# Performance work log

Hardware: AMD Instinct MI355X
Metric: run time of the kernel (lower is better)

The kernel has to match this reference:

```python
import jax, jax.numpy as jnp
import numpy as np

WINDOW = 512  # sliding-window size (keys per query, including self)


def setup_inputs() -> dict:
    key = jax.random.key(0)
    ks = jax.random.split(key, 5)
    B, T, C = 2, 8192, 1024
    s = 1.0 / np.sqrt(C)
    return {
        "x": jax.random.normal(ks[0], (B, T, C), dtype=jnp.float32),
        "Wq": jax.random.normal(ks[1], (C, C), dtype=jnp.float32) * s,
        "Wk": jax.random.normal(ks[2], (C, C), dtype=jnp.float32) * s,
        "Wv": jax.random.normal(ks[3], (C, C), dtype=jnp.float32) * s,
        "Wo": jax.random.normal(ks[4], (C, C), dtype=jnp.float32) * s,
    }


def _block_local_attn(q, k, v, window):
    # q,k,v: [B,H,T,D]; causal sliding-window attention, honoring sparsity by
    # attending only to the current and previous block of size `window`.
    B, H, T, D = q.shape
    W = window
    nb = T // W
    scale = 1.0 / jnp.sqrt(jnp.asarray(D, q.dtype))
    qb = q.reshape(B, H, nb, W, D)
    kb = k.reshape(B, H, nb, W, D)
    vb = v.reshape(B, H, nb, W, D)
    # previous block (zero-padded for block 0)
    kp = jnp.pad(kb, ((0, 0), (0, 0), (1, 0), (0, 0), (0, 0)))[:, :, :nb]
    vp = jnp.pad(vb, ((0, 0), (0, 0), (1, 0), (0, 0), (0, 0)))[:, :, :nb]
    k2 = jnp.concatenate([kp, kb], axis=3)  # [B,H,nb,2W,D]
    v2 = jnp.concatenate([vp, vb], axis=3)
    i = jnp.arange(W)[:, None]          # query index within block
    j = jnp.arange(2 * W)[None, :]      # key index (0..W-1 prev, W..2W-1 cur)
    # key global offset = j - W relative to query block start; causal window of
    # size W (self + W-1 previous) <=> i < j <= i + W
    base = (j > i) & (j <= i + W)                                  # [W,2W]
    prev_ok = (jnp.arange(nb)[:, None] > 0) | (jnp.arange(2 * W)[None, :] >= W)
    mask = base[None, :, :] & prev_ok[:, None, :]                  # [nb,W,2W]
    scores = jnp.einsum("bhnqd,bhnkd->bhnqk", qb, k2) * scale
    scores = jnp.where(mask[None, None], scores, jnp.asarray(-1e30, scores.dtype))
    p = jax.nn.softmax(scores, axis=-1)
    out = jnp.einsum("bhnqk,bhnkd->bhnqd", p, v2)
    return out.reshape(B, H, T, D)


def reference(x, Wq, Wk, Wv, Wo):
    B, T, C = x.shape
    H = 16
    D = C // H
    # nn.Linear(y = x @ W^T), bias=False
    q = (x @ Wq.T).reshape(B, T, H, D).transpose(0, 2, 1, 3)
    k = (x @ Wk.T).reshape(B, T, H, D).transpose(0, 2, 1, 3)
    v = (x @ Wv.T).reshape(B, T, H, D).transpose(0, 2, 1, 3)
    out = _block_local_attn(q, k, v, WINDOW)
    out = out.transpose(0, 2, 1, 3).reshape(B, T, C)
    return out @ Wo.T
```

## Files before the change

kernel.cpp:

```cpp
#include <hip/hip_runtime.h>
#include <hip/hip_bf16.h>
#include <stdint.h>

typedef __attribute__((ext_vector_type(8))) short short8;
typedef __attribute__((ext_vector_type(4))) float f32x4;
typedef __hip_bfloat16 bf16;

#define AS1 __attribute__((address_space(1)))
#define AS3 __attribute__((address_space(3)))

__device__ __forceinline__ void gl16(const void* g, void* l) {
  __builtin_amdgcn_global_load_lds((const AS1 unsigned int*)g,
                                   (AS3 unsigned int*)l, 16, 0, 0);
}

__device__ __forceinline__ unsigned short bfbits(float x) {
  union { bf16 b; unsigned short u; } c; c.b = __float2bfloat16(x); return c.u;
}

#define SCHED0 __builtin_amdgcn_sched_barrier(0)

__global__ __launch_bounds__(256) void k_cvt(const float* __restrict__ src,
                                             bf16* __restrict__ dst, int n8) {
  int i = blockIdx.x * blockDim.x + threadIdx.x;
  int stride = gridDim.x * blockDim.x;
  for (; i < n8; i += stride) {
    const float4* p = (const float4*)src + (size_t)i * 2;
    float4 a = p[0], b = p[1];
    bf16 tmp[8];
    tmp[0] = __float2bfloat16(a.x); tmp[1] = __float2bfloat16(a.y);
    tmp[2] = __float2bfloat16(a.z); tmp[3] = __float2bfloat16(a.w);
    tmp[4] = __float2bfloat16(b.x); tmp[5] = __float2bfloat16(b.y);
    tmp[6] = __float2bfloat16(b.z); tmp[7] = __float2bfloat16(b.w);
    *(short8*)(dst + (size_t)i * 8) = *(short8*)tmp;
  }
}

__global__ __launch_bounds__(256) void k_cvtw(
    const float* __restrict__ w0, const float* __restrict__ w1,
    const float* __restrict__ w2, const float* __restrict__ w3,
    bf16* __restrict__ d0, bf16* __restrict__ d1,
    bf16* __restrict__ d2, bf16* __restrict__ d3) {
  int gi = blockIdx.x * 256 + threadIdx.x;
  int m = gi >> 17;
  int i = gi & 131071;
  const float* src = (m == 0) ? w0 : (m == 1) ? w1 : (m == 2) ? w2 : w3;
  bf16* dst = (m == 0) ? d0 : (m == 1) ? d1 : (m == 2) ? d2 : d3;
  const float4* p = (const float4*)src + (size_t)i * 2;
  float4 a = p[0], b = p[1];
  bf16 tmp[8];
  tmp[0] = __float2bfloat16(a.x); tmp[1] = __float2bfloat16(a.y);
  tmp[2] = __float2bfloat16(a.z); tmp[3] = __float2bfloat16(a.w);
  tmp[4] = __float2bfloat16(b.x); tmp[5] = __float2bfloat16(b.y);
  tmp[6] = __float2bfloat16(b.z); tmp[7] = __float2bfloat16(b.w);
  *(short8*)(dst + (size_t)i * 8) = *(short8*)tmp;
}


#define GEMM_BODY(...)                                                         \
  const int Kd = 1024;                                                         \
  const int nk = 32;                                              \
  __shared__ bf16 As[4][256 * 32];                                             \
  __shared__ bf16 Bs[4][256 * 32];                                             \
  int tid = threadIdx.x;                                                       \
  int lane = tid & 63, wid = tid >> 6;                                         \
  int l15 = lane & 15, hi = lane >> 4;                                         \
  int wm = wid >> 2, wn = wid & 3;                                             \
  f32x4 acc[8][4];                                                             \
  _Pragma("unroll") for (int i = 0; i < 8; i++)                                \
      _Pragma("unroll") for (int j = 0; j < 4; j++)                            \
          acc[i][j] = (f32x4){0.f, 0.f, 0.f, 0.f};                             \
  auto stageA = [&](int slot, int kk) {                                        \
    const bf16* ab = Abase + kk * 32;                                          \
    _Pragma("unroll") for (int pass = 0; pass < 2; pass++) {                   \
      int p = pass * 512 + tid;                                                \
      int row = p >> 2;                                                        \
      int u = (p & 3) ^ ((row >> 1) & 3);                                      \
      gl16(ab + (size_t)row * Kd + u * 8, (char*)(&As[slot][0]) + p * 16);     \
    }                                                                          \
  };                                                                           \
  auto stageB = [&](int slot, int kk) {                                        \
    const bf16* bb = Bbase + kk * 32;                                          \
    _Pragma("unroll") for (int pass = 0; pass < 2; pass++) {                   \
      int p = pass * 512 + tid;                                                \
      int row = p >> 2;                                                        \
      int u = (p & 3) ^ ((row >> 1) & 3);                                      \
      gl16(bb + (size_t)row * Kd + u * 8, (char*)(&Bs[slot][0]) + p * 16);     \
    }                                                                          \
  };                                                                           \
  stageA(0, 0); stageB(0, 0);                                                  \
  stageA(1, 1); stageB(1, 1);                                                  \
  stageA(2, 2); stageB(2, 2);                                                  \
  asm volatile("s_waitcnt vmcnt(8)" ::: "memory");                             \
  SCHED0; __builtin_amdgcn_s_barrier(); SCHED0;                                \
  int sw = ((l15 >> 1) & 3) << 4;                                              \
  int arow = wm * 128 + l15;                                                   \
  int brow = wn * 64 + l15;                                                    \
  short8 ax[4], ahi[4], bcur[4], axn[4], bn[4];                                \
  _Pragma("unroll") for (int mf = 0; mf < 4; mf++)                             \
      ax[mf] = *(const short8*)((const char*)(&As[0][0]) +                     \
                                (((arow + mf * 16) * 64 + hi * 16) ^ sw));     \
  _Pragma("unroll") for (int nf = 0; nf < 4; nf++)                             \
      bcur[nf] = *(const short8*)((const char*)(&Bs[0][0]) +                   \
                                  (((brow + nf * 16) * 64 + hi * 16) ^ sw));   \
  _Pragma("unroll 2") for (int t = 0; t < nk; ++t) {                           \
    int s = t & 3, sn = (t + 1) & 3;                                           \
    const char* Ab = (const char*)(&As[s][0]);                                 \
    _Pragma("unroll") for (int mf = 0; mf < 4; mf++)                           \
        ahi[mf] = *(const short8*)(Ab +                                        \
            (((arow + 64 + mf * 16) * 64 + hi * 16) ^ sw));                    \
    if (t + 3 < nk) stageA((t + 3) & 3, t + 3);                                \
    SCHED0;                                                                    \
    __builtin_amdgcn_s_setprio(1);                                             \
    _Pragma("unroll") for (int mf = 0; mf < 4; mf++)                           \
        _Pragma("unroll") for (int nf = 0; nf < 4; nf++)                       \
            acc[mf][nf] = __builtin_amdgcn_mfma_f32_16x16x32_bf16(             \
                ax[mf], bcur[nf], acc[mf][nf], 0, 0, 0);                       \
    __builtin_amdgcn_s_setprio(0);                                             \
    SCHED0;                                                                    \
    if (t + 1 < nk) {                                                          \
      if (t + 3 < nk)      asm volatile("s_waitcnt vmcnt(6)" ::: "memory");    \
      else if (t + 2 < nk) asm volatile("s_waitcnt vmcnt(4)" ::: "memory");    \
      else                 asm volatile("s_waitcnt vmcnt(0)" ::: "memory");    \
      SCHED0; __builtin_amdgcn_s_barrier(); SCHED0;                            \
      if (t + 3 < nk) stageB((t + 3) & 3, t + 3);                              \
      const char* AbN = (const char*)(&As[sn][0]);                             \
      const char* BbN = (const char*)(&Bs[sn][0]);                             \
      _Pragma("unroll") for (int mf = 0; mf < 4; mf++)                         \
          axn[mf] = *(const short8*)(AbN +                                     \
              (((arow + mf * 16) * 64 + hi * 16) ^ sw));                       \
      _Pragma("unroll") for (int nf = 0; nf < 4; nf++)                         \
          bn[nf] = *(const short8*)(BbN +                                      \
              (((brow + nf * 16) * 64 + hi * 16) ^ sw));                       \
      SCHED0;                                                                  \
    }                                                                          \
    __builtin_amdgcn_s_setprio(1);                                             \
    _Pragma("unroll") for (int mf = 0; mf < 4; mf++)                           \
        _Pragma("unroll") for (int nf = 0; nf < 4; nf++)                       \
            acc[mf + 4][nf] = __builtin_amdgcn_mfma_f32_16x16x32_bf16(         \
                ahi[mf], bcur[nf], acc[mf + 4][nf], 0, 0, 0);                  \
    __builtin_amdgcn_s_setprio(0);                                             \
    SCHED0;                                                                    \
    if (t + 1 < nk) {                                                          \
      __builtin_amdgcn_s_barrier(); SCHED0;                                    \
      _Pragma("unroll") for (int i = 0; i < 4; i++) {                          \
        ax[i] = axn[i]; bcur[i] = bn[i];                                       \
      }                                                                        \
    }                                                                          \
  }                                                                            \
  __VA_ARGS__

__global__ __launch_bounds__(512, 2) void k_qkv_gemm(
    const bf16* __restrict__ X, const bf16* __restrict__ Wq,
    const bf16* __restrict__ Wk, const bf16* __restrict__ Wv,
    bf16* __restrict__ Q, bf16* __restrict__ K, bf16* __restrict__ V) {
  int bid = blockIdx.x;
  int wsel = bid >> 8;
  int rem = bid & 255;
  int mt = rem & 63;
  int nt = rem >> 6;
  const bf16* W = (wsel == 0) ? Wq : (wsel == 1) ? Wk : Wv;
  bf16* Dst = (wsel == 0) ? Q : (wsel == 1) ? K : V;
  const bf16* Abase = X + (size_t)mt * 256 * 1024;
  const bf16* Bbase = W + (size_t)nt * 256 * 1024;
  GEMM_BODY({
    _Pragma("unroll") for (int mf = 0; mf < 8; mf++) {
      _Pragma("unroll") for (int r = 0; r < 4; r++) {
        int row = mt * 256 + wm * 128 + mf * 16 + hi * 4 + r;
        int b = row >> 13;
        int tok = row & 8191;
        _Pragma("unroll") for (int nf = 0; nf < 4; nf++) {
          int col = nt * 256 + wn * 64 + nf * 16 + l15;
          int h = col >> 6;
          int d = col & 63;
          Dst[((size_t)(b * 16 + h) * 8192 + tok) * 64 + d] =
              __float2bfloat16(acc[mf][nf][r]);
        }
      }
    }
  })
}

__global__ __launch_bounds__(512, 2) void k_out_gemm(
    const bf16* __restrict__ A, const bf16* __restrict__ Wo,
    float* __restrict__ Out) {
  int bid = blockIdx.x;
  int mt = bid & 63;
  int nt = bid >> 6;
  const bf16* Abase = A + (size_t)mt * 256 * 1024;
  const bf16* Bbase = Wo + (size_t)nt * 256 * 1024;
  GEMM_BODY({
    _Pragma("unroll") for (int mf = 0; mf < 8; mf++) {
      _Pragma("unroll") for (int r = 0; r < 4; r++) {
        int row = mt * 256 + wm * 128 + mf * 16 + hi * 4 + r;
        _Pragma("unroll") for (int nf = 0; nf < 4; nf++) {
          int col = nt * 256 + wn * 64 + nf * 16 + l15;
          Out[(size_t)row * 1024 + col] = acc[mf][nf][r];
        }
      }
    }
  })
}

__global__ __launch_bounds__(256) void k_vtrans(const bf16* __restrict__ V,
                                                bf16* __restrict__ VT) {
  const int T = 8192;
  __shared__ bf16 tile[64][72];
  int bid = blockIdx.x;
  int tb = bid & 127;
  int bh = bid >> 7;
  int t0 = tb * 64;
  int tid = threadIdx.x;
  int r = tid >> 2, c4 = tid & 3;
  const bf16* src = V + ((size_t)bh * T + t0 + r) * 64 + c4 * 16;
  short8 a = *(const short8*)src;
  short8 b2 = *(const short8*)(src + 8);
#pragma unroll
  for (int e = 0; e < 8; e++) tile[r][c4 * 16 + e] = ((bf16*)&a)[e];
#pragma unroll
  for (int e = 0; e < 8; e++) tile[r][c4 * 16 + 8 + e] = ((bf16*)&b2)[e];
  __syncthreads();
  alignas(16) bf16 o[16];
#pragma unroll
  for (int e = 0; e < 16; e++) o[e] = tile[c4 * 16 + e][r];
  bf16* dst = VT + ((size_t)bh * 64 + r) * T + t0 + c4 * 16;
  *(short8*)dst = *(short8*)o;
  *(short8*)(dst + 8) = *((short8*)o + 1);
}

__global__ __launch_bounds__(512) void k_attn(
    const bf16* __restrict__ Q, const bf16* __restrict__ K,
    const bf16* __restrict__ VT, bf16* __restrict__ ATT) {
  const int T = 8192;
  __shared__ bf16 Ks[2][64 * 64];
  __shared__ bf16 Vs[2][64 * 64];
  __shared__ bf16 Ps[8][16 * 64];
  int bid = blockIdx.x;
  int qt = bid & 63;
  int bh = bid >> 6;
  int b = bh >> 4, h = bh & 15;
  int tid = threadIdx.x;
  int lane = tid & 63, wid = tid >> 6;
  int l15 = lane & 15, hi = lane >> 4;
  int q0 = qt * 128;
  int qw = q0 + wid * 16;

  short8 bq[2];
  const bf16* qp = Q + ((size_t)bh * T + qw + l15) * 64 + hi * 8;
  bq[0] = *(const short8*)qp;
  bq[1] = *(const short8*)(qp + 32);

  const bf16* Kbh = K + (size_t)bh * T * 64;
  const bf16* Vbh = VT + (size_t)bh * 64 * T;

  auto stage = [&](int bb, int c0) {
    int p = tid;
    int row = p >> 3;
    int u = (p & 7) ^ (row & 7);
    gl16(Kbh + ((size_t)(c0 + row)) * 64 + u * 8, (char*)(&Ks[bb][0]) + p * 16);
    gl16(Vbh + (size_t)row * T + c0 + u * 8, (char*)(&Vs[bb][0]) + p * 16);
  };

  int cstart = q0 - 512; if (cstart < 0) cstart = 0;
  int nch = (q0 + 128 - cstart) >> 6;

  f32x4 oacc[4];
#pragma unroll
  for (int c = 0; c < 4; c++) oacc[c] = (f32x4){0.f, 0.f, 0.f, 0.f};
  float ssum = 0.f;

  stage(0, cstart);
  __syncthreads();
  int buf = 0;
  for (int ci = 0; ci < nch; ci++) {
    int c0 = cstart + (ci << 6);
    if (ci + 1 < nch) stage(buf ^ 1, c0 + 64);
    f32x4 sacc[4];
#pragma unroll
    for (int ks = 0; ks < 4; ks++) sacc[ks] = (f32x4){0.f, 0.f, 0.f, 0.f};
#pragma unroll
    for (int dh = 0; dh < 2; dh++) {
#pragma unroll
      for (int ks = 0; ks < 4; ks++) {
        int krow = ks * 16 + l15;
        int boff = ((krow * 64 + dh * 32 + hi * 8) * 2) ^ ((krow & 7) << 4);
        short8 ak = *(const short8*)((const char*)(&Ks[buf][0]) + boff);
        sacc[ks] = __builtin_amdgcn_mfma_f32_16x16x32_bf16(ak, bq[dh], sacc[ks], 0, 0, 0);
      }
    }
    float pv[4][4];
    float psum = 0.f;
    bool fullok = (c0 + 63 <= qw) && (c0 + 512 >= qw + 16);
    if (fullok) {
#pragma unroll
      for (int ks = 0; ks < 4; ks++)
#pragma unroll
        for (int r = 0; r < 4; r++) {
          float p = __expf(fmaf(sacc[ks][r], 0.125f, -12.0f));
          pv[ks][r] = p;
          psum += p;
        }
    } else {
      int qg = qw + l15;
#pragma unroll
      for (int ks = 0; ks < 4; ks++)
#pragma unroll
        for (int r = 0; r < 4; r++) {
          int jg = c0 + ks * 16 + hi * 4 + r;
          float p = __expf(fmaf(sacc[ks][r], 0.125f, -12.0f));
          p = ((jg <= qg) && (jg > qg - 512)) ? p : 0.f;
          pv[ks][r] = p;
          psum += p;
        }
    }
    psum += __shfl_xor(psum, 16);
    psum += __shfl_xor(psum, 32);
    ssum += psum;
#pragma unroll
    for (int ks = 0; ks < 4; ks++) {
      unsigned int lo = (unsigned)bfbits(pv[ks][0]) | ((unsigned)bfbits(pv[ks][1]) << 16);
      unsigned int hi2 = (unsigned)bfbits(pv[ks][2]) | ((unsigned)bfbits(pv[ks][3]) << 16);
      int j0 = ks * 16 + hi * 4;
      int a0 = ((l15 * 64 + j0) * 2) ^ ((l15 & 7) << 4);
      int a1 = ((l15 * 64 + j0 + 2) * 2) ^ ((l15 & 7) << 4);
      *(unsigned int*)((char*)(&Ps[wid][0]) + a0) = lo;
      *(unsigned int*)((char*)(&Ps[wid][0]) + a1) = hi2;
    }
    short8 ap[2];
#pragma unroll
    for (int js = 0; js < 2; js++) {
      int a = ((l15 * 64 + js * 32 + hi * 8) * 2) ^ ((l15 & 7) << 4);
      ap[js] = *(const short8*)((const char*)(&Ps[wid][0]) + a);
    }
#pragma unroll
    for (int js = 0; js < 2; js++)
#pragma unroll
      for (int c = 0; c < 4; c++) {
        int vrow = c * 16 + l15;
        int boff = ((vrow * 64 + js * 32 + hi * 8) * 2) ^ ((vrow & 7) << 4);
        short8 bv = *(const short8*)((const char*)(&Vs[buf][0]) + boff);
        oacc[c] = __builtin_amdgcn_mfma_f32_16x16x32_bf16(ap[js], bv, oacc[c], 0, 0, 0);
      }
    __syncthreads();
    buf ^= 1;
  }
  float inv = 1.f / ssum;
#pragma unroll
  for (int r = 0; r < 4; r++) {
    float f = __shfl(inv, hi * 4 + r);
    int tok = qw + hi * 4 + r;
    bf16* dst = ATT + ((size_t)b * 8192 + tok) * 1024 + h * 64;
#pragma unroll
    for (int c = 0; c < 4; c++)
      dst[c * 16 + l15] = __float2bfloat16(oacc[c][r] * f);
  }
}

extern "C" void kernel_launch(void* const* d_in, const int* in_sizes, int n_in,
                              void* d_out, int out_size, void* d_ws, size_t ws_size,
                              hipStream_t stream) {
  const float* x  = (const float*)d_in[0];
  const float* wq = (const float*)d_in[1];
  const float* wk = (const float*)d_in[2];
  const float* wv = (const float*)d_in[3];
  const float* wo = (const float*)d_in[4];
  float* out = (float*)d_out;

  char* ws = (char*)d_ws;
  const size_t SZ_X = (size_t)16384 * 1024 * 2;
  const size_t SZ_W = (size_t)1024 * 1024 * 2;
  size_t off = 0;
  bf16* xb  = (bf16*)(ws + off); off += SZ_X;
  bf16* wqb = (bf16*)(ws + off); off += SZ_W;
  bf16* wkb = (bf16*)(ws + off); off += SZ_W;
  bf16* wvb = (bf16*)(ws + off); off += SZ_W;
  bf16* wob = (bf16*)(ws + off); off += SZ_W;
  bf16* qb  = (bf16*)(ws + off); off += SZ_X;
  bf16* kb  = (bf16*)(ws + off); off += SZ_X;
  bf16* vb  = (bf16*)(ws + off); off += SZ_X;
  bf16* vtb = (bf16*)(ws + off); off += SZ_X;
  bf16* att = xb;

  k_cvt<<<2048, 256, 0, stream>>>(x, xb, 16384 * 1024 / 8);
  k_cvtw<<<2048, 256, 0, stream>>>(wq, wk, wv, wo, wqb, wkb, wvb, wob);
  k_qkv_gemm<<<768, 512, 0, stream>>>(xb, wqb, wkb, wvb, qb, kb, vb);
  k_vtrans<<<4096, 256, 0, stream>>>(vb, vtb);
  k_attn<<<2048, 512, 0, stream>>>(qb, kb, vtb, att);
  k_out_gemm<<<256, 512, 0, stream>>>(att, wob, out);
}
```

Baseline: 283.5 us.

## Shrink GEMM tiles to 128x256 with simpler double-buffered pipeline

Result: no change. 287.1 us (+1.3%).

```diff
diff --git a/kernel.cpp b/kernel.cpp
--- a/kernel.cpp
+++ b/kernel.cpp
@@ -60,113 +60,82 @@
 #define GEMM_BODY(...)                                                         \
   const int Kd = 1024;                                                         \
   const int nk = 32;                                              \
-  __shared__ bf16 As[4][256 * 32];                                             \
-  __shared__ bf16 Bs[4][256 * 32];                                             \
+  __shared__ bf16 As[2][128 * 32];                                             \
+  __shared__ bf16 Bs[2][256 * 32];                                             \
   int tid = threadIdx.x;                                                       \
   int lane = tid & 63, wid = tid >> 6;                                         \
   int l15 = lane & 15, hi = lane >> 4;                                         \
   int wm = wid >> 2, wn = wid & 3;                                             \
-  f32x4 acc[8][4];                                                             \
-  _Pragma("unroll") for (int i = 0; i < 8; i++)                                \
+  f32x4 acc[4][4];                                                             \
+  _Pragma("unroll") for (int i = 0; i < 4; i++)                                \
       _Pragma("unroll") for (int j = 0; j < 4; j++)                            \
           acc[i][j] = (f32x4){0.f, 0.f, 0.f, 0.f};                             \
-  auto stageA = [&](int slot, int kk) {                                        \
+  auto stage = [&](int slot, int kk) {                                         \
     const bf16* ab = Abase + kk * 32;                                          \
-    _Pragma("unroll") for (int pass = 0; pass < 2; pass++) {                   \
-      int p = pass * 512 + tid;                                                \
+    const bf16* bb = Bbase + kk * 32;                                          \
+    {                                                                          \
+      int p = tid;                      \
       int row = p >> 2;                                                        \
       int u = (p & 3) ^ ((row >> 1) & 3);                                      \
       gl16(ab + (size_t)row * Kd + u * 8, (char*)(&As[slot][0]) + p * 16);     \
     }                                                                          \
-  };                                                                           \
-  auto stageB = [&](int slot, int kk) {                                        \
-    const bf16* bb = Bbase + kk * 32;                                          \
     _Pragma("unroll") for (int pass = 0; pass < 2; pass++) {                   \
-      int p = pass * 512 + tid;                                                \
+      int p = pass * 512 + tid;             \
       int row = p >> 2;                                                        \
       int u = (p & 3) ^ ((row >> 1) & 3);                                      \
       gl16(bb + (size_t)row * Kd + u * 8, (char*)(&Bs[slot][0]) + p * 16);     \
     }                                                                          \
   };                                                                           \
-  stageA(0, 0); stageB(0, 0);                                                  \
-  stageA(1, 1); stageB(1, 1);                                                  \
-  stageA(2, 2); stageB(2, 2);                                                  \
-  asm volatile("s_waitcnt vmcnt(8)" ::: "memory");                             \
+  stage(0, 0);                                                                 \
+  asm volatile("s_waitcnt vmcnt(0)" ::: "memory");                             \
   SCHED0; __builtin_amdgcn_s_barrier(); SCHED0;                                \
   int sw = ((l15 >> 1) & 3) << 4;                                              \
-  int arow = wm * 128 + l15;                                                   \
+  int arow = wm * 64 + l15;                                                    \
   int brow = wn * 64 + l15;                                                    \
-  short8 ax[4], ahi[4], bcur[4], axn[4], bn[4];                                \
-  _Pragma("unroll") for (int mf = 0; mf < 4; mf++)                             \
-      ax[mf] = *(const short8*)((const char*)(&As[0][0]) +                     \
-                                (((arow + mf * 16) * 64 + hi * 16) ^ sw));     \
-  _Pragma("unroll") for (int nf = 0; nf < 4; nf++)                             \
-      bcur[nf] = *(const short8*)((const char*)(&Bs[0][0]) +                   \
-                                  (((brow + nf * 16) * 64 + hi * 16) ^ sw));   \
   _Pragma("unroll 2") for (int t = 0; t < nk; ++t) {                           \
-    int s = t & 3, sn = (t + 1) & 3;                                           \
+    int s = t & 1;                                                             \
     const char* Ab = (const char*)(&As[s][0]);                                 \
+    const char* Bb = (const char*)(&Bs[s][0]);                                 \
+    if (t + 1 < nk) stage(s ^ 1, t + 1);                                       \
+    short8 af[4], bfr[4];                                                      \
     _Pragma("unroll") for (int mf = 0; mf < 4; mf++)                           \
-        ahi[mf] = *(const short8*)(Ab +                                        \
-            (((arow + 64 + mf * 16) * 64 + hi * 16) ^ sw));                    \
-    if (t + 3 < nk) stageA((t + 3) & 3, t + 3);                                \
+        af[mf] = *(const short8*)(Ab +                                         \
+            (((arow + mf * 16) * 64 + hi * 16) ^ sw));                         \
+    _Pragma("unroll") for (int nf = 0; nf < 4; nf++)                           \
+        bfr[nf] = *(const short8*)(Bb +                                        \
+            (((brow + nf * 16) * 64 + hi * 16) ^ sw));                         \
     SCHED0;                                                                    \
     __builtin_amdgcn_s_setprio(1);                                             \
     _Pragma("unroll") for (int mf = 0; mf < 4; mf++)                           \
         _Pragma("unroll") for (int nf = 0; nf < 4; nf++)                       \
             acc[mf][nf] = __builtin_amdgcn_mfma_f32_16x16x32_bf16(             \
-                ax[mf], bcur[nf], acc[mf][nf], 0, 0, 0);                       \
+                af[mf], bfr[nf], acc[mf][nf], 0, 0, 0);                        \
     __builtin_amdgcn_s_setprio(0);                                             \
     SCHED0;                                                                    \
     if (t + 1 < nk) {                                                          \
-      if (t + 3 < nk)      asm volatile("s_waitcnt vmcnt(6)" ::: "memory");    \
-      else if (t + 2 < nk) asm volatile("s_waitcnt vmcnt(4)" ::: "memory");    \
-      else                 asm volatile("s_waitcnt vmcnt(0)" ::: "memory");    \
+      asm volatile("s_waitcnt vmcnt(0)" ::: "memory");                         \
       SCHED0; __builtin_amdgcn_s_barrier(); SCHED0;                            \
-      if (t + 3 < nk) stageB((t + 3) & 3, t + 3);                              \
-      const char* AbN = (const char*)(&As[sn][0]);                             \
-      const char* BbN = (const char*)(&Bs[sn][0]);                             \
-      _Pragma("unroll") for (int mf = 0; mf < 4; mf++)                         \
-          axn[mf] = *(const short8*)(AbN +                                     \
-              (((arow + mf * 16) * 64 + hi * 16) ^ sw));                       \
-      _Pragma("unroll") for (int nf = 0; nf < 4; nf++)                         \
-          bn[nf] = *(const short8*)(BbN +                                      \
-              (((brow + nf * 16) * 64 + hi * 16) ^ sw));                       \
-      SCHED0;                                                                  \
-    }                                                                          \
-    __builtin_amdgcn_s_setprio(1);                                             \
-    _Pragma("unroll") for (int mf = 0; mf < 4; mf++)                           \
-        _Pragma("unroll") for (int nf = 0; nf < 4; nf++)                       \
-            acc[mf + 4][nf] = __builtin_amdgcn_mfma_f32_16x16x32_bf16(         \
-                ahi[mf], bcur[nf], acc[mf + 4][nf], 0, 0, 0);                  \
-    __builtin_amdgcn_s_setprio(0);                                             \
-    SCHED0;                                                                    \
-    if (t + 1 < nk) {                                                          \
-      __builtin_amdgcn_s_barrier(); SCHED0;                                    \
-      _Pragma("unroll") for (int i = 0; i < 4; i++) {                          \
-        ax[i] = axn[i]; bcur[i] = bn[i];                                       \
-      }                                                                        \
     }                                                                          \
   }                                                                            \
   __VA_ARGS__
 
-__global__ __launch_bounds__(512, 2) void k_qkv_gemm(
+__global__ __launch_bounds__(512, 4) void k_qkv_gemm(
     const bf16* __restrict__ X, const bf16* __restrict__ Wq,
     const bf16* __restrict__ Wk, const bf16* __restrict__ Wv,
     bf16* __restrict__ Q, bf16* __restrict__ K, bf16* __restrict__ V) {
   int bid = blockIdx.x;
-  int wsel = bid >> 8;
-  int rem = bid & 255;
-  int mt = rem & 63;
-  int nt = rem >> 6;
+  int wsel = bid >> 9;
+  int rem = bid & 511;
+  int mt = rem & 127;
+  int nt = rem >> 7;
   const bf16* W = (wsel == 0) ? Wq : (wsel == 1) ? Wk : Wv;
   bf16* Dst = (wsel == 0) ? Q : (wsel == 1) ? K : V;
-  const bf16* Abase = X + (size_t)mt * 256 * 1024;
+  const bf16* Abase = X + (size_t)mt * 128 * 1024;
   const bf16* Bbase = W + (size_t)nt * 256 * 1024;
   GEMM_BODY({
-    _Pragma("unroll") for (int mf = 0; mf < 8; mf++) {
+    _Pragma("unroll") for (int mf = 0; mf < 4; mf++) {
       _Pragma("unroll") for (int r = 0; r < 4; r++) {
-        int row = mt * 256 + wm * 128 + mf * 16 + hi * 4 + r;
+        int row = mt * 128 + wm * 64 + mf * 16 + hi * 4 + r;
         int b = row >> 13;
         int tok = row & 8191;
         _Pragma("unroll") for (int nf = 0; nf < 4; nf++) {
@@ -181,18 +150,18 @@
   })
 }
 
-__global__ __launch_bounds__(512, 2) void k_out_gemm(
+__global__ __launch_bounds__(512, 4) void k_out_gemm(
     const bf16* __restrict__ A, const bf16* __restrict__ Wo,
     float* __restrict__ Out) {
   int bid = blockIdx.x;
-  int mt = bid & 63;
-  int nt = bid >> 6;
-  const bf16* Abase = A + (size_t)mt * 256 * 1024;
+  int mt = bid & 127;
+  int nt = bid >> 7;
+  const bf16* Abase = A + (size_t)mt * 128 * 1024;
   const bf16* Bbase = Wo + (size_t)nt * 256 * 1024;
   GEMM_BODY({
-    _Pragma("unroll") for (int mf = 0; mf < 8; mf++) {
+    _Pragma("unroll") for (int mf = 0; mf < 4; mf++) {
       _Pragma("unroll") for (int r = 0; r < 4; r++) {
-        int row = mt * 256 + wm * 128 + mf * 16 + hi * 4 + r;
+        int row = mt * 128 + wm * 64 + mf * 16 + hi * 4 + r;
         _Pragma("unroll") for (int nf = 0; nf < 4; nf++) {
           int col = nt * 256 + wn * 64 + nf * 16 + l15;
           Out[(size_t)row * 1024 + col] = acc[mf][nf][r];
@@ -383,8 +352,8 @@
 
   k_cvt<<<2048, 256, 0, stream>>>(x, xb, 16384 * 1024 / 8);
   k_cvtw<<<2048, 256, 0, stream>>>(wq, wk, wv, wo, wqb, wkb, wvb, wob);
-  k_qkv_gemm<<<768, 512, 0, stream>>>(xb, wqb, wkb, wvb, qb, kb, vb);
+  k_qkv_gemm<<<1536, 512, 0, stream>>>(xb, wqb, wkb, wvb, qb, kb, vb);
   k_vtrans<<<4096, 256, 0, stream>>>(vb, vtb);
   k_attn<<<2048, 512, 0, stream>>>(qb, kb, vtb, att);
-  k_out_gemm<<<256, 512, 0, stream>>>(att, wob, out);
-}
+  k_out_gemm<<<512, 512, 0, stream>>>(att, wob, out);
+}
```

## Use 128x256 tiles with double buffering for QKV GEMM

Applied to the files above, without the earlier changes.

Measured after the change: 278.1 us. About the same (-1.9%).

```diff
diff --git a/kernel.cpp b/kernel.cpp
--- a/kernel.cpp
+++ b/kernel.cpp
@@ -57,9 +57,72 @@
 }
 
 
-#define GEMM_BODY(...)                                                         \
+#define GEMM_BODY128(...)                                                      \
   const int Kd = 1024;                                                         \
-  const int nk = 32;                                              \
+  const int nk = 32;                                                           \
+  __shared__ bf16 As[2][128 * 32];                                             \
+  __shared__ bf16 Bs[2][256 * 32];                                             \
+  int tid = threadIdx.x;                                                       \
+  int lane = tid & 63, wid = tid >> 6;                                         \
+  int l15 = lane & 15, hi = lane >> 4;                                         \
+  int wm = wid >> 2, wn = wid & 3;                                             \
+  f32x4 acc[4][4];                                                             \
+  _Pragma("unroll") for (int i = 0; i < 4; i++)                                \
+      _Pragma("unroll") for (int j = 0; j < 4; j++)                            \
+          acc[i][j] = (f32x4){0.f, 0.f, 0.f, 0.f};                             \
+  auto stage = [&](int slot, int kk) {                                         \
+    const bf16* ab = Abase + kk * 32;                                          \
+    const bf16* bb = Bbase + kk * 32;                                          \
+    {                                                                          \
+      int p = tid;                                                             \
+      int row = p >> 2;                                                        \
+      int u = (p & 3) ^ ((row >> 1) & 3);                                      \
+      gl16(ab + (size_t)row * Kd + u * 8, (char*)(&As[slot][0]) + p * 16);     \
+    }                                                                          \
+    _Pragma("unroll") for (int pass = 0; pass < 2; pass++) {                   \
+      int p = pass * 512 + tid;                                                \
+      int row = p >> 2;                                                        \
+      int u = (p & 3) ^ ((row >> 1) & 3);                                      \
+      gl16(bb + (size_t)row * Kd + u * 8, (char*)(&Bs[slot][0]) + p * 16);     \
+    }                                                                          \
+  };                                                                           \
+  stage(0, 0);                                                                 \
+  asm volatile("s_waitcnt vmcnt(0)" ::: "memory");                             \
+  SCHED0; __builtin_amdgcn_s_barrier(); SCHED0;                                \
+  int sw = ((l15 >> 1) & 3) << 4;                                              \
+  int arow = wm * 64 + l15;                                                    \
+  int brow = wn * 64 + l15;                                                    \
+  _Pragma("unroll 2") for (int t = 0; t < nk; ++t) {                           \
+    int s = t & 1;                                                             \
+    const char* Ab = (const char*)(&As[s][0]);                                 \
+    const char* Bb = (const char*)(&Bs[s][0]);                                 \
+    if (t + 1 < nk) stage(s ^ 1, t + 1);                                       \
+    short8 af[4], bfr[4];                                                      \
+    _Pragma("unroll") for (int mf = 0; mf < 4; mf++)                           \
+        af[mf] = *(const short8*)(Ab +                                         \
+            (((arow + mf * 16) * 64 + hi * 16) ^ sw));                         \
+    _Pragma("unroll") for (int nf = 0; nf < 4; nf++)                           \
+        bfr[nf] = *(const short8*)(Bb +                                        \
+            (((brow + nf * 16) * 64 + hi * 16) ^ sw));                         \
+    SCHED0;                                                                    \
+    __builtin_amdgcn_s_setprio(1);                                             \
+    _Pragma("unroll") for (int mf = 0; mf < 4; mf++)                           \
+        _Pragma("unroll") for (int nf = 0; nf < 4; nf++)                       \
+            acc[mf][nf] = __builtin_amdgcn_mfma_f32_16x16x32_bf16(             \
+                af[mf], bfr[nf], acc[mf][nf], 0, 0, 0);                        \
+    __builtin_amdgcn_s_setprio(0);                                             \
+    SCHED0;                                                                    \
+    if (t + 1 < nk) {                                                          \
+      asm volatile("s_waitcnt vmcnt(0)" ::: "memory");                         \
+      SCHED0; __builtin_amdgcn_s_barrier(); SCHED0;                            \
+    }                                                                          \
+  }                                                                            \
+  __VA_ARGS__
+
+
+#define GEMM_BODY256(...)                                                      \
+  const int Kd = 1024;                                                         \
+  const int nk = 32;                                                           \
   __shared__ bf16 As[4][256 * 32];                                             \
   __shared__ bf16 Bs[4][256 * 32];                                             \
   int tid = threadIdx.x;                                                       \
@@ -150,23 +213,23 @@
   }                                                                            \
   __VA_ARGS__
 
-__global__ __launch_bounds__(512, 2) void k_qkv_gemm(
+__global__ __launch_bounds__(512, 4) void k_qkv_gemm(
     const bf16* __restrict__ X, const bf16* __restrict__ Wq,
     const bf16* __restrict__ Wk, const bf16* __restrict__ Wv,
     bf16* __restrict__ Q, bf16* __restrict__ K, bf16* __restrict__ V) {
   int bid = blockIdx.x;
-  int wsel = bid >> 8;
-  int rem = bid & 255;
-  int mt = rem & 63;
-  int nt = rem >> 6;
+  int wsel = bid >> 9;
+  int rem = bid & 511;
+  int mt = rem & 127;
+  int nt = rem >> 7;
   const bf16* W = (wsel == 0) ? Wq : (wsel == 1) ? Wk : Wv;
   bf16* Dst = (wsel == 0) ? Q : (wsel == 1) ? K : V;
-  const bf16* Abase = X + (size_t)mt * 256 * 1024;
+  const bf16* Abase = X + (size_t)mt * 128 * 1024;
   const bf16* Bbase = W + (size_t)nt * 256 * 1024;
-  GEMM_BODY({
-    _Pragma("unroll") for (int mf = 0; mf < 8; mf++) {
+  GEMM_BODY128({
+    _Pragma("unroll") for (int mf = 0; mf < 4; mf++) {
       _Pragma("unroll") for (int r = 0; r < 4; r++) {
-        int row = mt * 256 + wm * 128 + mf * 16 + hi * 4 + r;
+        int row = mt * 128 + wm * 64 + mf * 16 + hi * 4 + r;
         int b = row >> 13;
         int tok = row & 8191;
         _Pragma("unroll") for (int nf = 0; nf < 4; nf++) {
@@ -189,7 +252,7 @@
   int nt = bid >> 6;
   const bf16* Abase = A + (size_t)mt * 256 * 1024;
   const bf16* Bbase = Wo + (size_t)nt * 256 * 1024;
-  GEMM_BODY({
+  GEMM_BODY256({
     _Pragma("unroll") for (int mf = 0; mf < 8; mf++) {
       _Pragma("unroll") for (int r = 0; r < 4; r++) {
         int row = mt * 256 + wm * 128 + mf * 16 + hi * 4 + r;
@@ -383,7 +446,7 @@
 
   k_cvt<<<2048, 256, 0, stream>>>(x, xb, 16384 * 1024 / 8);
   k_cvtw<<<2048, 256, 0, stream>>>(wq, wk, wv, wo, wqb, wkb, wvb, wob);
-  k_qkv_gemm<<<768, 512, 0, stream>>>(xb, wqb, wkb, wvb, qb, kb, vb);
+  k_qkv_gemm<<<1536, 512, 0, stream>>>(xb, wqb, wkb, wvb, qb, kb, vb);
   k_vtrans<<<4096, 256, 0, stream>>>(vb, vtb);
   k_attn<<<2048, 512, 0, stream>>>(qb, kb, vtb, att);
   k_out_gemm<<<256, 512, 0, stream>>>(att, wob, out);
```
